# Kernel optimization log

Measured on AMD Instinct MI355X. Metric: run time of the kernel, lower is better.

Reference implementation:

```python
import jax, jax.numpy as jnp
import numpy as np
import math

EPS = 1e-8
NUM_FREQS = 64
NUM_BINS = 128
NUM_QUERIES = 32768
HEAD_DIM = NUM_FREQS * 2


def setup_inputs() -> dict:
    key = jax.random.key(0)
    k1, k2, k3, k4, k5 = jax.random.split(key, 5)
    init_value = math.log(math.e - 1.0)
    return {
        "Q": jax.random.normal(k1, (NUM_QUERIES, HEAD_DIM), dtype=jnp.float32),
        "rotated_probes": jax.random.normal(k2, (NUM_BINS, HEAD_DIM), dtype=jnp.float32),
        # faithful init is full(init_value); add small noise so grads are non-degenerate
        "q_weights_raw": init_value + 0.1 * jax.random.normal(k3, (NUM_BINS, NUM_FREQS), dtype=jnp.float32),
        "q_magnitude_weights": 0.1 * jax.random.normal(k4, (NUM_BINS, NUM_FREQS), dtype=jnp.float32),
        "q_bias": 0.1 * jax.random.normal(k5, (NUM_BINS,), dtype=jnp.float32),
    }


def reference(Q, rotated_probes, q_weights_raw, q_magnitude_weights, q_bias):
    F = NUM_FREQS
    # L2-normalize queries (use_l2_norm=True)
    Qn = Q / (jnp.linalg.norm(Q, axis=-1, keepdims=True) + EPS)  # (q, d)
    Q_real, Q_imag = Qn[:, :F], Qn[:, F:]                        # (q, f)
    P_real, P_imag = rotated_probes[:, :F], rotated_probes[:, F:]  # (b, f)
    # per-frequency complex error and distance: (q, b, f)
    error_real = P_real[None, :, :] - Q_real[:, None, :]
    error_imag = P_imag[None, :, :] - Q_imag[:, None, :]
    distance = jnp.sqrt(error_real ** 2 + error_imag ** 2 + EPS)
    # per-frequency magnitude of normalized Q: (q, f)
    Q_magnitude = jnp.sqrt(Q_real ** 2 + Q_imag ** 2 + EPS)
    # negative weights via softplus
    effective_weights = -jax.nn.softplus(q_weights_raw)          # (b, f)
    distance_term = jnp.einsum('qbf,bf->qb', distance, effective_weights)
    magnitude_term = Q_magnitude @ q_magnitude_weights.T          # (q, b)
    scores = distance_term + magnitude_term + q_bias[None, :]
    return scores
```

## Files before the change

### kernel.cpp

```cpp
#include <hip/hip_runtime.h>
#include <math.h>

#define NUM_FREQS   64
#define NUM_BINS    128
#define NUM_QUERIES 32768
#define HEAD_DIM    128
#define EPS         1e-8f
#define NQB         32

__global__ void prep_fused(const float* __restrict__ Q,
                           const float* __restrict__ rp,
                           const float* __restrict__ wraw,
                           const float* __restrict__ mw,
                           float2* __restrict__ Qri,
                           float*  __restrict__ Qm,
                           float4* __restrict__ probe4) {
    const int bid = blockIdx.x;
    const int tid = threadIdx.x;
    if (bid < 128) {
        int q = bid * 256 + tid;
        const float4* Qrow = reinterpret_cast<const float4*>(Q + (size_t)q * HEAD_DIM);
        float4 buf[32];
        float s = 0.0f;
        #pragma unroll
        for (int i = 0; i < 32; i++) {
            float4 v = Qrow[i];
            buf[i] = v;
            s = fmaf(v.x, v.x, fmaf(v.y, v.y, fmaf(v.z, v.z, fmaf(v.w, v.w, s))));
        }
        float inv = 1.0f / (__builtin_amdgcn_sqrtf(s) + EPS);
        #pragma unroll
        for (int i = 0; i < 16; i++) {
            float4 r  = buf[i];
            float4 im = buf[16 + i];
            float rr[4] = { r.x,  r.y,  r.z,  r.w  };
            float ii[4] = { im.x, im.y, im.z, im.w };
            #pragma unroll
            for (int k = 0; k < 4; k++) {
                float qr = rr[k] * inv;
                float qi = ii[k] * inv;
                float qm = __builtin_amdgcn_sqrtf(fmaf(qr, qr, fmaf(qi, qi, EPS)));
                int f = 4 * i + k;
                Qri[(size_t)f * NUM_QUERIES + q] = make_float2(qr, qi);
                Qm [(size_t)f * NUM_QUERIES + q] = qm;
            }
        }
    } else {
        int idx = (bid - 128) * 256 + tid;
        if (idx >= NUM_FREQS * NUM_BINS) return;
        int f = idx >> 7;
        int b = idx & 127;
        float pr = rp[b * HEAD_DIM + f];
        float pi = rp[b * HEAD_DIM + NUM_FREQS + f];
        float w  = wraw[b * NUM_FREQS + f];
        float sp = fmaxf(w, 0.0f) + log1pf(expf(-fabsf(w)));
        float m  = mw[b * NUM_FREQS + f];
        probe4[idx] = make_float4(pr, pi, -sp, m);
    }
}

__global__ __launch_bounds__(256, 4) void main_kernel(
        const float4* __restrict__ probe4,
        const float2* __restrict__ Qri,
        const float*  __restrict__ Qm,
        const float*  __restrict__ bias,
        float*        __restrict__ out) {
    __shared__ float2 qri[NUM_FREQS + 1][NQB];
    __shared__ float  qmv[NUM_FREQS + 1][NQB];

    const int tid   = threadIdx.x;
    const int qbase = blockIdx.x * NQB;

    #pragma unroll
    for (int i = 0; i < (NUM_FREQS * NQB) / 256; i++) {
        int idx = i * 256 + tid;
        int f = idx >> 5, j = idx & 31;
        qri[f][j] = Qri[(size_t)f * NUM_QUERIES + qbase + j];
        qmv[f][j] = Qm [(size_t)f * NUM_QUERIES + qbase + j];
    }
    __syncthreads();

    const int lane = tid & 63;
    const int wave = tid >> 6;
    const int jb   = wave * 8;

    float acc0[8], acc1[8];
    #pragma unroll
    for (int j = 0; j < 8; j++) { acc0[j] = 0.0f; acc1[j] = 0.0f; }

    const float4* pp = probe4 + lane;
    const float4* aq = reinterpret_cast<const float4*>(&qri[0][jb]);
    const float4* mq = reinterpret_cast<const float4*>(&qmv[0][jb]);

    float4 P0 = pp[0], P1 = pp[64];
    float4 a0 = aq[0], a1 = aq[1], a2 = aq[2], a3 = aq[3];
    float4 m0 = mq[0], m1 = mq[1];

    #pragma unroll 4
    for (int f = 0; f < NUM_FREQS; f++) {
        const float4* ppn = pp + NUM_BINS;
        float4 P0n = ppn[0],  P1n = ppn[64];
        const float4* aqn = aq + 16;
        const float4* mqn = mq + 8;
        float4 a0n = aqn[0], a1n = aqn[1], a2n = aqn[2], a3n = aqn[3];
        float4 m0n = mqn[0], m1n = mqn[1];

        const float mmv[8] = { m0.x, m0.y, m0.z, m0.w,  m1.x, m1.y, m1.z, m1.w };
        const float4 av[4] = { a0, a1, a2, a3 };
        #pragma unroll
        for (int k = 0; k < 4; k++) {
            float4 a = av[k];
            {
                float er0 = P0.x - a.x, ei0 = P0.y - a.y;
                float d0  = __builtin_amdgcn_sqrtf(fmaf(er0, er0, fmaf(ei0, ei0, EPS)));
                acc0[2*k] = fmaf(d0, P0.z, fmaf(mmv[2*k], P0.w, acc0[2*k]));
                float er1 = P1.x - a.x, ei1 = P1.y - a.y;
                float d1  = __builtin_amdgcn_sqrtf(fmaf(er1, er1, fmaf(ei1, ei1, EPS)));
                acc1[2*k] = fmaf(d1, P1.z, fmaf(mmv[2*k], P1.w, acc1[2*k]));
            }
            {
                float er0 = P0.x - a.z, ei0 = P0.y - a.w;
                float d0  = __builtin_amdgcn_sqrtf(fmaf(er0, er0, fmaf(ei0, ei0, EPS)));
                acc0[2*k+1] = fmaf(d0, P0.z, fmaf(mmv[2*k+1], P0.w, acc0[2*k+1]));
                float er1 = P1.x - a.z, ei1 = P1.y - a.w;
                float d1  = __builtin_amdgcn_sqrtf(fmaf(er1, er1, fmaf(ei1, ei1, EPS)));
                acc1[2*k+1] = fmaf(d1, P1.z, fmaf(mmv[2*k+1], P1.w, acc1[2*k+1]));
            }
        }

        P0 = P0n; P1 = P1n;
        a0 = a0n; a1 = a1n; a2 = a2n; a3 = a3n;
        m0 = m0n; m1 = m1n;
        pp = ppn; aq = aqn; mq = mqn;
    }

    float b0 = bias[lane];
    float b1 = bias[64 + lane];
    #pragma unroll
    for (int j = 0; j < 8; j++) {
        size_t row = (size_t)(qbase + jb + j) * NUM_BINS;
        out[row + lane]      = acc0[j] + b0;
        out[row + 64 + lane] = acc1[j] + b1;
    }
}

__global__ void fallback_kernel(const float* __restrict__ Q,
                                const float* __restrict__ rp,
                                const float* __restrict__ wraw,
                                const float* __restrict__ mw,
                                const float* __restrict__ bias,
                                float* __restrict__ out) {
    __shared__ float qn[HEAD_DIM];
    __shared__ float qmag[NUM_FREQS];
    __shared__ float red[NUM_BINS];
    const int t = threadIdx.x;
    const int q = blockIdx.x;

    float v = Q[(size_t)q * HEAD_DIM + t];
    red[t] = v * v;
    __syncthreads();
    for (int s = 64; s > 0; s >>= 1) {
        if (t < s) red[t] += red[t + s];
        __syncthreads();
    }
    float inv = 1.0f / (__builtin_amdgcn_sqrtf(red[0]) + EPS);
    qn[t] = v * inv;
    __syncthreads();
    if (t < NUM_FREQS) {
        float a = qn[t], c = qn[t + NUM_FREQS];
        qmag[t] = __builtin_amdgcn_sqrtf(fmaf(a, a, fmaf(c, c, EPS)));
    }
    __syncthreads();

    const int b = t;
    float acc = 0.0f;
    for (int f = 0; f < NUM_FREQS; f++) {
        float pr = rp[(size_t)b * HEAD_DIM + f];
        float pi = rp[(size_t)b * HEAD_DIM + NUM_FREQS + f];
        float w  = wraw[(size_t)b * NUM_FREQS + f];
        float ew = -(fmaxf(w, 0.0f) + log1pf(expf(-fabsf(w))));
        float er = pr - qn[f];
        float ei = pi - qn[f + NUM_FREQS];
        float d  = __builtin_amdgcn_sqrtf(fmaf(er, er, fmaf(ei, ei, EPS)));
        acc = fmaf(d, ew, fmaf(qmag[f], mw[(size_t)b * NUM_FREQS + f], acc));
    }
    out[(size_t)q * NUM_BINS + b] = acc + bias[b];
}

extern "C" void kernel_launch(void* const* d_in, const int* in_sizes, int n_in,
                              void* d_out, int out_size, void* d_ws, size_t ws_size,
                              hipStream_t stream) {
    const float* Q    = (const float*)d_in[0];
    const float* rp   = (const float*)d_in[1];
    const float* wraw = (const float*)d_in[2];
    const float* mw   = (const float*)d_in[3];
    const float* bias = (const float*)d_in[4];
    float* out = (float*)d_out;

    const size_t probeBytes = (size_t)NUM_FREQS * NUM_BINS * sizeof(float4);
    const size_t qriBytes   = (size_t)NUM_FREQS * NUM_QUERIES * sizeof(float2);
    const size_t qmBytes    = (size_t)NUM_FREQS * NUM_QUERIES * sizeof(float);
    const size_t need       = probeBytes + qriBytes + qmBytes;

    if (ws_size >= need) {
        float4* probe4 = (float4*)d_ws;
        float2* Qri    = (float2*)((char*)d_ws + probeBytes);
        float*  Qm     = (float*)((char*)d_ws + probeBytes + qriBytes);

        hipLaunchKernelGGL(prep_fused, dim3(128 + 32), dim3(256), 0, stream,
                           Q, rp, wraw, mw, Qri, Qm, probe4);
        hipLaunchKernelGGL(main_kernel, dim3(NUM_QUERIES / NQB), dim3(256), 0,
                           stream, probe4, Qri, Qm, bias, out);
    } else {
        hipLaunchKernelGGL(fallback_kernel, dim3(NUM_QUERIES), dim3(NUM_BINS), 0,
                           stream, Q, rp, wraw, mw, bias, out);
    }
}
```

Before: 74.73 us.

## Use packed FP32 math with bit-hack rsqrt and split real/imag planes

```diff
diff --git a/kernel.cpp b/kernel.cpp
--- a/kernel.cpp
+++ b/kernel.cpp
@@ -8,12 +8,57 @@
 #define EPS         1e-8f
 #define NQB         32
 
+typedef float v2f __attribute__((ext_vector_type(2)));
+
+__device__ __forceinline__ v2f pk_add(v2f a, v2f b) {
+    v2f d;
+    asm("v_pk_add_f32 %0, %1, %2" : "=v"(d) : "v"(a), "v"(b));
+    return d;
+}
+__device__ __forceinline__ v2f pk_mul(v2f a, v2f b) {
+    v2f d;
+    asm("v_pk_mul_f32 %0, %1, %2" : "=v"(d) : "v"(a), "v"(b));
+    return d;
+}
+__device__ __forceinline__ v2f pk_fma(v2f a, v2f b, v2f c) {
+    v2f d;
+    asm("v_pk_fma_f32 %0, %1, %2, %3" : "=v"(d) : "v"(a), "v"(b), "v"(c));
+    return d;
+}
+
+__device__ __forceinline__ v2f pk_rsqrt_guess(v2f s) {
+    int il = 0x5f375a86 - (__float_as_int(s.x) >> 1);
+    int ih = 0x5f375a86 - (__float_as_int(s.y) >> 1);
+    v2f r;
+    r.x = __int_as_float(il);
+    r.y = __int_as_float(ih);
+    return r;
+}
+
+__device__ __forceinline__ v2f slot(v2f prd, v2f pid, v2f wzd, v2f mwd,
+                                    v2f nqr, v2f nqi, v2f qm2, v2f acc,
+                                    v2f eps2, v2f nhalf, v2f c15) {
+    v2f er = pk_add(prd, nqr);
+    v2f ei = pk_add(pid, nqi);
+    v2f t  = pk_fma(ei, ei, eps2);
+    v2f s  = pk_fma(er, er, t);
+    v2f r0 = pk_rsqrt_guess(s);
+    v2f nxh = pk_mul(s, nhalf);
+    v2f u   = pk_mul(nxh, r0);
+    v2f w   = pk_fma(u, r0, c15);
+    v2f r1  = pk_mul(r0, w);
+    v2f d   = pk_mul(s, r1);
+    v2f a   = pk_fma(qm2, mwd, acc);
+    return pk_fma(d, wzd, a);
+}
+
 __global__ void prep_fused(const float* __restrict__ Q,
                            const float* __restrict__ rp,
                            const float* __restrict__ wraw,
                            const float* __restrict__ mw,
-                           float2* __restrict__ Qri,
-                           float*  __restrict__ Qm,
+                           float* __restrict__ Qnr,
+                           float* __restrict__ Qni,
+                           float* __restrict__ Qm,
                            float4* __restrict__ probe4) {
     const int bid = blockIdx.x;
     const int tid = threadIdx.x;
@@ -41,7 +86,8 @@
                 float qi = ii[k] * inv;
                 float qm = __builtin_amdgcn_sqrtf(fmaf(qr, qr, fmaf(qi, qi, EPS)));
                 int f = 4 * i + k;
-                Qri[(size_t)f * NUM_QUERIES + q] = make_float2(qr, qi);
+                Qnr[(size_t)f * NUM_QUERIES + q] = -qr;
+                Qni[(size_t)f * NUM_QUERIES + q] = -qi;
                 Qm [(size_t)f * NUM_QUERIES + q] = qm;
             }
         }
@@ -61,86 +107,86 @@
 
 __global__ __launch_bounds__(256, 4) void main_kernel(
         const float4* __restrict__ probe4,
-        const float2* __restrict__ Qri,
+        const float*  __restrict__ Qnr,
+        const float*  __restrict__ Qni,
         const float*  __restrict__ Qm,
         const float*  __restrict__ bias,
         float*        __restrict__ out) {
-    __shared__ float2 qri[NUM_FREQS + 1][NQB];
-    __shared__ float  qmv[NUM_FREQS + 1][NQB];
+    __shared__ float snr[NUM_FREQS * NQB];
+    __shared__ float sni[NUM_FREQS * NQB];
+    __shared__ float sqm[NUM_FREQS * NQB];
 
     const int tid   = threadIdx.x;
     const int qbase = blockIdx.x * NQB;
 
     #pragma unroll
-    for (int i = 0; i < (NUM_FREQS * NQB) / 256; i++) {
+    for (int i = 0; i < 2; i++) {
         int idx = i * 256 + tid;
-        int f = idx >> 5, j = idx & 31;
-        qri[f][j] = Qri[(size_t)f * NUM_QUERIES + qbase + j];
-        qmv[f][j] = Qm [(size_t)f * NUM_QUERIES + qbase + j];
+        int f = idx >> 3, j4 = idx & 7;
+        const float4* gr = reinterpret_cast<const float4*>(Qnr + (size_t)f * NUM_QUERIES + qbase);
+        const float4* gi = reinterpret_cast<const float4*>(Qni + (size_t)f * NUM_QUERIES + qbase);
+        const float4* gm = reinterpret_cast<const float4*>(Qm  + (size_t)f * NUM_QUERIES + qbase);
+        reinterpret_cast<float4*>(snr)[f * 8 + j4] = gr[j4];
+        reinterpret_cast<float4*>(sni)[f * 8 + j4] = gi[j4];
+        reinterpret_cast<float4*>(sqm)[f * 8 + j4] = gm[j4];
     }
     __syncthreads();
 
     const int lane = tid & 63;
     const int wave = tid >> 6;
-    const int jb   = wave * 8;
-
-    float acc0[8], acc1[8];
+
+    const v2f eps2  = { EPS, EPS };
+    const v2f nhalf = { -0.5f, -0.5f };
+    const v2f c15   = { 1.5f, 1.5f };
+
+    v2f acc[4][2];
     #pragma unroll
-    for (int j = 0; j < 8; j++) { acc0[j] = 0.0f; acc1[j] = 0.0f; }
+    for (int p = 0; p < 4; p++) {
+        acc[p][0] = (v2f){0.0f, 0.0f};
+        acc[p][1] = (v2f){0.0f, 0.0f};
+    }
 
     const float4* pp = probe4 + lane;
-    const float4* aq = reinterpret_cast<const float4*>(&qri[0][jb]);
-    const float4* mq = reinterpret_cast<const float4*>(&qmv[0][jb]);
-
-    float4 P0 = pp[0], P1 = pp[64];
-    float4 a0 = aq[0], a1 = aq[1], a2 = aq[2], a3 = aq[3];
-    float4 m0 = mq[0], m1 = mq[1];
-
-    #pragma unroll 4
+    const float4* ar = reinterpret_cast<const float4*>(snr) + wave * 2;
+    const float4* ai = reinterpret_cast<const float4*>(sni) + wave * 2;
+    const float4* am = reinterpret_cast<const float4*>(sqm) + wave * 2;
+
+    #pragma unroll 2
     for (int f = 0; f < NUM_FREQS; f++) {
-        const float4* ppn = pp + NUM_BINS;
-        float4 P0n = ppn[0],  P1n = ppn[64];
-        const float4* aqn = aq + 16;
-        const float4* mqn = mq + 8;
-        float4 a0n = aqn[0], a1n = aqn[1], a2n = aqn[2], a3n = aqn[3];
-        float4 m0n = mqn[0], m1n = mqn[1];
-
-        const float mmv[8] = { m0.x, m0.y, m0.z, m0.w,  m1.x, m1.y, m1.z, m1.w };
-        const float4 av[4] = { a0, a1, a2, a3 };
+        float4 P0 = pp[0];
+        float4 P1 = pp[64];
+        float4 R0 = ar[0], R1 = ar[1];
+        float4 I0 = ai[0], I1 = ai[1];
+        float4 M0 = am[0], M1 = am[1];
+        pp += NUM_BINS; ar += 8; ai += 8; am += 8;
+
+        v2f pr0 = {P0.x, P0.x}, pi0 = {P0.y, P0.y}, wz0 = {P0.z, P0.z}, mw0 = {P0.w, P0.w};
+        v2f pr1 = {P1.x, P1.x}, pi1 = {P1.y, P1.y}, wz1 = {P1.z, P1.z}, mw1 = {P1.w, P1.w};
+
+        const v2f nr[4] = { {R0.x, R0.y}, {R0.z, R0.w}, {R1.x, R1.y}, {R1.z, R1.w} };
+        const v2f ni[4] = { {I0.x, I0.y}, {I0.z, I0.w}, {I1.x, I1.y}, {I1.z, I1.w} };
+        const v2f qm2[4] = { {M0.x, M0.y}, {M0.z, M0.w}, {M1.x, M1.y}, {M1.z, M1.w} };
+
         #pragma unroll
-        for (int k = 0; k < 4; k++) {
-            float4 a = av[k];
-            {
-                float er0 = P0.x - a.x, ei0 = P0.y - a.y;
-                float d0  = __builtin_amdgcn_sqrtf(fmaf(er0, er0, fmaf(ei0, ei0, EPS)));
-                acc0[2*k] = fmaf(d0, P0.z, fmaf(mmv[2*k], P0.w, acc0[2*k]));
-                float er1 = P1.x - a.x, ei1 = P1.y - a.y;
-                float d1  = __builtin_amdgcn_sqrtf(fmaf(er1, er1, fmaf(ei1, ei1, EPS)));
-                acc1[2*k] = fmaf(d1, P1.z, fmaf(mmv[2*k], P1.w, acc1[2*k]));
-            }
-            {
-                float er0 = P0.x - a.z, ei0 = P0.y - a.w;
-                float d0  = __builtin_amdgcn_sqrtf(fmaf(er0, er0, fmaf(ei0, ei0, EPS)));
-                acc0[2*k+1] = fmaf(d0, P0.z, fmaf(mmv[2*k+1], P0.w, acc0[2*k+1]));
-                float er1 = P1.x - a.z, ei1 = P1.y - a.w;
-                float d1  = __builtin_amdgcn_sqrtf(fmaf(er1, er1, fmaf(ei1, ei1, EPS)));
-                acc1[2*k+1] = fmaf(d1, P1.z, fmaf(mmv[2*k+1], P1.w, acc1[2*k+1]));
-            }
+        for (int p = 0; p < 4; p++) {
+            acc[p][0] = slot(pr0, pi0, wz0, mw0, nr[p], ni[p], qm2[p], acc[p][0],
+                             eps2, nhalf, c15);
+            acc[p][1] = slot(pr1, pi1, wz1, mw1, nr[p], ni[p], qm2[p], acc[p][1],
+                             eps2, nhalf, c15);
         }
-
-        P0 = P0n; P1 = P1n;
-        a0 = a0n; a1 = a1n; a2 = a2n; a3 = a3n;
-        m0 = m0n; m1 = m1n;
-        pp = ppn; aq = aqn; mq = mqn;
-    }
-
+    }
+
+    const int jb = wave * 8;
     float b0 = bias[lane];
     float b1 = bias[64 + lane];
     #pragma unroll
-    for (int j = 0; j < 8; j++) {
-        size_t row = (size_t)(qbase + jb + j) * NUM_BINS;
-        out[row + lane]      = acc0[j] + b0;
-        out[row + 64 + lane] = acc1[j] + b1;
+    for (int p = 0; p < 4; p++) {
+        size_t r0 = (size_t)(qbase + jb + 2 * p) * NUM_BINS;
+        size_t r1 = r0 + NUM_BINS;
+        out[r0 + lane]      = acc[p][0].x + b0;
+        out[r1 + lane]      = acc[p][0].y + b0;
+        out[r0 + 64 + lane] = acc[p][1].x + b1;
+        out[r1 + 64 + lane] = acc[p][1].y + b1;
     }
 }
 
@@ -198,19 +244,19 @@
     float* out = (float*)d_out;
 
     const size_t probeBytes = (size_t)NUM_FREQS * NUM_BINS * sizeof(float4);
-    const size_t qriBytes   = (size_t)NUM_FREQS * NUM_QUERIES * sizeof(float2);
-    const size_t qmBytes    = (size_t)NUM_FREQS * NUM_QUERIES * sizeof(float);
-    const size_t need       = probeBytes + qriBytes + qmBytes;
+    const size_t planeBytes = (size_t)NUM_FREQS * NUM_QUERIES * sizeof(float);
+    const size_t need       = probeBytes + 3 * planeBytes;
 
     if (ws_size >= need) {
         float4* probe4 = (float4*)d_ws;
-        float2* Qri    = (float2*)((char*)d_ws + probeBytes);
-        float*  Qm     = (float*)((char*)d_ws + probeBytes + qriBytes);
+        float*  Qnr    = (float*)((char*)d_ws + probeBytes);
+        float*  Qni    = Qnr + (size_t)NUM_FREQS * NUM_QUERIES;
+        float*  Qm     = Qni + (size_t)NUM_FREQS * NUM_QUERIES;
 
         hipLaunchKernelGGL(prep_fused, dim3(128 + 32), dim3(256), 0, stream,
-                           Q, rp, wraw, mw, Qri, Qm, probe4);
+                           Q, rp, wraw, mw, Qnr, Qni, Qm, probe4);
         hipLaunchKernelGGL(main_kernel, dim3(NUM_QUERIES / NQB), dim3(256), 0,
-                           stream, probe4, Qri, Qm, bias, out);
+                           stream, probe4, Qnr, Qni, Qm, bias, out);
     } else {
         hipLaunchKernelGGL(fallback_kernel, dim3(NUM_QUERIES), dim3(NUM_BINS), 0,
                            stream, Q, rp, wraw, mw, bias, out);
```

New measurement: 91.42 us. +22.3%, slower.

## Expand squared distance algebraically and halve query tile for higher occupancy

Applied to the files above, without the earlier changes.

```diff
diff --git a/kernel.cpp b/kernel.cpp
--- a/kernel.cpp
+++ b/kernel.cpp
@@ -6,7 +6,7 @@
 #define NUM_QUERIES 32768
 #define HEAD_DIM    128
 #define EPS         1e-8f
-#define NQB         32
+#define NQB         16
 
 __global__ void prep_fused(const float* __restrict__ Q,
                            const float* __restrict__ rp,
@@ -14,7 +14,8 @@
                            const float* __restrict__ mw,
                            float2* __restrict__ Qri,
                            float*  __restrict__ Qm,
-                           float4* __restrict__ probe4) {
+                           float4* __restrict__ probeA,
+                           float*  __restrict__ probeM) {
     const int bid = blockIdx.x;
     const int tid = threadIdx.x;
     if (bid < 128) {
@@ -54,93 +55,94 @@
         float pi = rp[b * HEAD_DIM + NUM_FREQS + f];
         float w  = wraw[b * NUM_FREQS + f];
         float sp = fmaxf(w, 0.0f) + log1pf(expf(-fabsf(w)));
-        float m  = mw[b * NUM_FREQS + f];
-        probe4[idx] = make_float4(pr, pi, -sp, m);
-    }
-}
-
-__global__ __launch_bounds__(256, 4) void main_kernel(
-        const float4* __restrict__ probe4,
+        probeA[idx] = make_float4(-2.0f * pr, -2.0f * pi,
+                                  fmaf(pr, pr, pi * pi), -sp);
+        probeM[idx] = mw[b * NUM_FREQS + f];
+    }
+}
+
+__global__ __launch_bounds__(256, 8) void main_kernel(
+        const float4* __restrict__ probeA,
+        const float*  __restrict__ probeM,
         const float2* __restrict__ Qri,
         const float*  __restrict__ Qm,
         const float*  __restrict__ bias,
         float*        __restrict__ out) {
-    __shared__ float2 qri[NUM_FREQS + 1][NQB];
-    __shared__ float  qmv[NUM_FREQS + 1][NQB];
+    __shared__ float2 sri[NUM_FREQS][NQB];
+    __shared__ float  sqm[NUM_FREQS][NQB];
 
     const int tid   = threadIdx.x;
     const int qbase = blockIdx.x * NQB;
 
     #pragma unroll
-    for (int i = 0; i < (NUM_FREQS * NQB) / 256; i++) {
+    for (int i = 0; i < 3; i++) {
         int idx = i * 256 + tid;
-        int f = idx >> 5, j = idx & 31;
-        qri[f][j] = Qri[(size_t)f * NUM_QUERIES + qbase + j];
-        qmv[f][j] = Qm [(size_t)f * NUM_QUERIES + qbase + j];
+        if (idx < 512) {
+            int f = idx >> 3, c = idx & 7;
+            reinterpret_cast<float4*>(&sri[f][0])[c] =
+                reinterpret_cast<const float4*>(Qri + (size_t)f * NUM_QUERIES + qbase)[c];
+        } else {
+            int t2 = idx - 512;
+            int f = t2 >> 2, c = t2 & 3;
+            reinterpret_cast<float4*>(&sqm[f][0])[c] =
+                reinterpret_cast<const float4*>(Qm + (size_t)f * NUM_QUERIES + qbase)[c];
+        }
     }
     __syncthreads();
 
     const int lane = tid & 63;
     const int wave = tid >> 6;
-    const int jb   = wave * 8;
-
-    float acc0[8], acc1[8];
+    const int jb   = wave * 4;
+
+    float acc0[4], acc1[4];
     #pragma unroll
-    for (int j = 0; j < 8; j++) { acc0[j] = 0.0f; acc1[j] = 0.0f; }
-
-    const float4* pp = probe4 + lane;
-    const float4* aq = reinterpret_cast<const float4*>(&qri[0][jb]);
-    const float4* mq = reinterpret_cast<const float4*>(&qmv[0][jb]);
-
-    float4 P0 = pp[0], P1 = pp[64];
-    float4 a0 = aq[0], a1 = aq[1], a2 = aq[2], a3 = aq[3];
-    float4 m0 = mq[0], m1 = mq[1];
+    for (int p = 0; p < 4; p++) { acc0[p] = 0.0f; acc1[p] = 0.0f; }
+
+    const float4* pA = probeA + lane;
+    const float*  pM = probeM + lane;
 
     #pragma unroll 4
     for (int f = 0; f < NUM_FREQS; f++) {
-        const float4* ppn = pp + NUM_BINS;
-        float4 P0n = ppn[0],  P1n = ppn[64];
-        const float4* aqn = aq + 16;
-        const float4* mqn = mq + 8;
-        float4 a0n = aqn[0], a1n = aqn[1], a2n = aqn[2], a3n = aqn[3];
-        float4 m0n = mqn[0], m1n = mqn[1];
-
-        const float mmv[8] = { m0.x, m0.y, m0.z, m0.w,  m1.x, m1.y, m1.z, m1.w };
-        const float4 av[4] = { a0, a1, a2, a3 };
+        float4 P0 = pA[0];
+        float4 P1 = pA[64];
+        float  w0 = pM[0];
+        float  w1 = pM[64];
+        float4 r01 = *reinterpret_cast<const float4*>(&sri[f][jb]);
+        float4 r23 = *reinterpret_cast<const float4*>(&sri[f][jb + 2]);
+        float4 qm4 = *reinterpret_cast<const float4*>(&sqm[f][jb]);
+        pA += NUM_BINS; pM += NUM_BINS;
+
+        const float qrv[4] = { r01.x, r01.z, r23.x, r23.z };
+        const float qiv[4] = { r01.y, r01.w, r23.y, r23.w };
+        const float qmv[4] = { qm4.x, qm4.y, qm4.z, qm4.w };
+
         #pragma unroll
-        for (int k = 0; k < 4; k++) {
-            float4 a = av[k];
+        for (int p = 0; p < 4; p++) {
+            float qr = qrv[p], qi = qiv[p], qm = qmv[p];
             {
-                float er0 = P0.x - a.x, ei0 = P0.y - a.y;
-                float d0  = __builtin_amdgcn_sqrtf(fmaf(er0, er0, fmaf(ei0, ei0, EPS)));
-                acc0[2*k] = fmaf(d0, P0.z, fmaf(mmv[2*k], P0.w, acc0[2*k]));
-                float er1 = P1.x - a.x, ei1 = P1.y - a.y;
-                float d1  = __builtin_amdgcn_sqrtf(fmaf(er1, er1, fmaf(ei1, ei1, EPS)));
-                acc1[2*k] = fmaf(d1, P1.z, fmaf(mmv[2*k], P1.w, acc1[2*k]));
+                float a = fmaf(qm, qm, P0.z);
+                a = fmaf(P0.x, qr, a);
+                a = fmaf(P0.y, qi, a);
+                float d = __builtin_amdgcn_sqrtf(a);
+                acc0[p] = fmaf(d, P0.w, fmaf(qm, w0, acc0[p]));
             }
             {
-                float er0 = P0.x - a.z, ei0 = P0.y - a.w;
-                float d0  = __builtin_amdgcn_sqrtf(fmaf(er0, er0, fmaf(ei0, ei0, EPS)));
-                acc0[2*k+1] = fmaf(d0, P0.z, fmaf(mmv[2*k+1], P0.w, acc0[2*k+1]));
-                float er1 = P1.x - a.z, ei1 = P1.y - a.w;
-                float d1  = __builtin_amdgcn_sqrtf(fmaf(er1, er1, fmaf(ei1, ei1, EPS)));
-                acc1[2*k+1] = fmaf(d1, P1.z, fmaf(mmv[2*k+1], P1.w, acc1[2*k+1]));
+                float a = fmaf(qm, qm, P1.z);
+                a = fmaf(P1.x, qr, a);
+                a = fmaf(P1.y, qi, a);
+                float d = __builtin_amdgcn_sqrtf(a);
+                acc1[p] = fmaf(d, P1.w, fmaf(qm, w1, acc1[p]));
             }
         }
-
-        P0 = P0n; P1 = P1n;
-        a0 = a0n; a1 = a1n; a2 = a2n; a3 = a3n;
-        m0 = m0n; m1 = m1n;
-        pp = ppn; aq = aqn; mq = mqn;
     }
 
     float b0 = bias[lane];
     float b1 = bias[64 + lane];
     #pragma unroll
-    for (int j = 0; j < 8; j++) {
-        size_t row = (size_t)(qbase + jb + j) * NUM_BINS;
-        out[row + lane]      = acc0[j] + b0;
-        out[row + 64 + lane] = acc1[j] + b1;
+    for (int p = 0; p < 4; p++) {
+        size_t row = (size_t)(qbase + jb + p) * NUM_BINS;
+        out[row + lane]      = acc0[p] + b0;
+        out[row + 64 + lane] = acc1[p] + b1;
     }
 }
 
@@ -197,20 +199,22 @@
     const float* bias = (const float*)d_in[4];
     float* out = (float*)d_out;
 
-    const size_t probeBytes = (size_t)NUM_FREQS * NUM_BINS * sizeof(float4);
-    const size_t qriBytes   = (size_t)NUM_FREQS * NUM_QUERIES * sizeof(float2);
-    const size_t qmBytes    = (size_t)NUM_FREQS * NUM_QUERIES * sizeof(float);
-    const size_t need       = probeBytes + qriBytes + qmBytes;
+    const size_t pABytes  = (size_t)NUM_FREQS * NUM_BINS * sizeof(float4);
+    const size_t pMBytes  = (size_t)NUM_FREQS * NUM_BINS * sizeof(float);
+    const size_t qriBytes = (size_t)NUM_FREQS * NUM_QUERIES * sizeof(float2);
+    const size_t qmBytes  = (size_t)NUM_FREQS * NUM_QUERIES * sizeof(float);
+    const size_t need     = pABytes + pMBytes + qriBytes + qmBytes;
 
     if (ws_size >= need) {
-        float4* probe4 = (float4*)d_ws;
-        float2* Qri    = (float2*)((char*)d_ws + probeBytes);
-        float*  Qm     = (float*)((char*)d_ws + probeBytes + qriBytes);
+        float4* probeA = (float4*)d_ws;
+        float*  probeM = (float*)((char*)d_ws + pABytes);
+        float2* Qri    = (float2*)((char*)d_ws + pABytes + pMBytes);
+        float*  Qm     = (float*)((char*)d_ws + pABytes + pMBytes + qriBytes);
 
         hipLaunchKernelGGL(prep_fused, dim3(128 + 32), dim3(256), 0, stream,
-                           Q, rp, wraw, mw, Qri, Qm, probe4);
+                           Q, rp, wraw, mw, Qri, Qm, probeA, probeM);
         hipLaunchKernelGGL(main_kernel, dim3(NUM_QUERIES / NQB), dim3(256), 0,
-                           stream, probe4, Qri, Qm, bias, out);
+                           stream, probeA, probeM, Qri, Qm, bias, out);
     } else {
         hipLaunchKernelGGL(fallback_kernel, dim3(NUM_QUERIES), dim3(NUM_BINS), 0,
                            stream, Q, rp, wraw, mw, bias, out);
```

New measurement: 78.46 us. +5.0%, slower.
